# Optimization experiments

Measured on AMD Instinct MI355X. Metric: run time of the kernel, lower is better.

## Reference

```python
import jax, jax.numpy as jnp
import numpy as np


def setup_inputs() -> dict:
    key = jax.random.key(0)
    ks = jax.random.split(key, 9)
    B, C, O, T, H, W = 2, 256, 256, 16, 64, 64
    fea_th = jax.random.normal(ks[0], (B, C, T, H), dtype=jnp.float32)
    fea_tw = jax.random.normal(ks[1], (B, C, T, W), dtype=jnp.float32)
    fea_obj = jax.random.normal(ks[2], (B, C, T), dtype=jnp.float32)
    heatmap = jax.random.uniform(ks[3], (B, 1, T, H, W), dtype=jnp.float32)
    mask = jax.random.uniform(ks[4], (B, 1, T, H, W), dtype=jnp.float32)
    s = 1.0 / np.sqrt(C)
    W3d = jax.random.uniform(ks[5], (O, C), dtype=jnp.float32, minval=-s, maxval=s)
    b3d = jax.random.uniform(ks[6], (O,), dtype=jnp.float32, minval=-s, maxval=s)
    W1d = jax.random.uniform(ks[7], (O, C), dtype=jnp.float32, minval=-s, maxval=s)
    b1d = jax.random.uniform(ks[8], (O,), dtype=jnp.float32, minval=-s, maxval=s)
    return {"fea_th": fea_th, "fea_tw": fea_tw, "fea_obj": fea_obj,
            "heatmap": heatmap, "mask": mask,
            "W3d": W3d, "b3d": b3d, "W1d": W1d, "b1d": b1d}


def reference(fea_th, fea_tw, fea_obj, heatmap, mask, W3d, b3d, W1d, b1d):
    # Outer product over spatial dims: [B,C,T,H,1] * [B,C,T,1,W] -> [B,C,T,H,W]
    out_fea = fea_th[..., None] * fea_tw[..., None, :]
    # 1x1x1 Conv3d == channel mixing: bcthw,oc -> bothw (+ bias)
    out_fea = jnp.einsum('bcthw,oc->bothw', out_fea, W3d) + b3d[None, :, None, None, None]
    # 1x1 Conv1d on fea_obj: bct,oc -> bot (+ bias), then broadcast over H,W
    fea_obj_ = (jnp.einsum('bct,oc->bot', fea_obj, W1d) + b1d[None, :, None])[..., None, None]
    # Heatmap blend and mask
    out_fea = out_fea * (1.0 - heatmap) + fea_obj_ * heatmap
    out_fea = out_fea * mask
    return out_fea
```

## Files before the change

### kernel.cpp

```cpp
#include <hip/hip_runtime.h>
#include <hip/hip_bf16.h>

#define B_ 2
#define C_ 256
#define O_ 256
#define T_ 16
#define H_ 64
#define W_ 64

typedef __bf16 bf16x8 __attribute__((ext_vector_type(8)));
typedef float  f32x4  __attribute__((ext_vector_type(4)));

#define WS_OBJ_OFF 131072

__global__ __launch_bounds__(256) void prep_kernel(
    const float* __restrict__ fea_obj, const float* __restrict__ W3d,
    const float* __restrict__ W1d, const float* __restrict__ b1d,
    __bf16* __restrict__ wsW, float* __restrict__ wsObj) {
    const int bid = blockIdx.x;
    const int tid = threadIdx.x;
    if (bid < 32) {
        const int b = bid >> 4, t = bid & 15;
        __shared__ float fo[C_];
        fo[tid] = fea_obj[(b * C_ + tid) * T_ + t];
        __syncthreads();
        const int o = tid;
        const float4* wrow = (const float4*)(W1d + o * C_);
        float s = 0.f;
#pragma unroll 8
        for (int cq = 0; cq < C_ / 4; ++cq) {
            float4 wv = wrow[cq];
            s += wv.x * fo[cq * 4 + 0] + wv.y * fo[cq * 4 + 1] +
                 wv.z * fo[cq * 4 + 2] + wv.w * fo[cq * 4 + 3];
        }
        wsObj[(b * T_ + t) * O_ + o] = s + b1d[o];
    } else {
        const int g = (bid - 32) * 256 + tid;
        const int o = g >> 5;
        const int cg = g & 31;
        const float* sp = W3d + o * C_ + cg * 8;
        float4 a0 = *(const float4*)sp;
        float4 a1 = *(const float4*)(sp + 4);
        bf16x8 pk;
        pk[0] = (__bf16)a0.x; pk[1] = (__bf16)a0.y;
        pk[2] = (__bf16)a0.z; pk[3] = (__bf16)a0.w;
        pk[4] = (__bf16)a1.x; pk[5] = (__bf16)a1.y;
        pk[6] = (__bf16)a1.z; pk[7] = (__bf16)a1.w;
        *(bf16x8*)((char*)wsW + o * 512 + cg * 16) = pk;
    }
}

__global__ __attribute__((amdgpu_flat_work_group_size(512, 512)))
void main_kernel(
    const float* __restrict__ fea_th, const float* __restrict__ fea_tw,
    const float* __restrict__ heatmap, const float* __restrict__ mask,
    const float* __restrict__ b3d,
    const __bf16* __restrict__ wsW, const float* __restrict__ wsObj,
    float* __restrict__ out) {
    __shared__ __align__(16) char smem[43008];
    char*  sB0  = smem;
    char*  sB1  = smem + 16384;
    float* sTh  = (float*)(smem + 32768);
    float* sPb  = (float*)(smem + 40960);
    float* sObj = (float*)(smem + 41984);

    const int tid  = threadIdx.x;
    const int lane = tid & 63;
    const int wv   = tid >> 6;
    const int kgrp = lane >> 4;
    const int l15  = lane & 15;

    const int bid = blockIdx.x;
    const int wb = bid & 1, hg = (bid >> 1) & 7, bt = bid >> 4;
    const int b = bt >> 4, t = bt & 15;
    const int h0 = hg * 8, w0 = wb * 32;

    const float* objp = wsObj + (b * T_ + t) * O_;
    if (tid < 256) {
        const float* thp = fea_th + ((b * C_ + tid) * T_ + t) * H_ + h0;
        float4 v0 = *(const float4*)thp;
        float4 v1 = *(const float4*)(thp + 4);
        sTh[0 * 256 + tid] = v0.x;  sTh[1 * 256 + tid] = v0.y;
        sTh[2 * 256 + tid] = v0.z;  sTh[3 * 256 + tid] = v0.w;
        sTh[4 * 256 + tid] = v1.x;  sTh[5 * 256 + tid] = v1.y;
        sTh[6 * 256 + tid] = v1.z;  sTh[7 * 256 + tid] = v1.w;
        sPb[tid]  = b3d[tid];
        sObj[tid] = objp[tid];
    }

    const int wl = tid & 31;
    const int cs = (tid >> 5) * 16;
    bf16x8 twb0, twb1;
    {
        const float* twp = fea_tw + ((b * C_ + cs) * T_ + t) * W_ + w0 + wl;
#pragma unroll
        for (int j = 0; j < 8; ++j) twb0[j] = (__bf16)twp[j * (T_ * W_)];
#pragma unroll
        for (int j = 0; j < 8; ++j) twb1[j] = (__bf16)twp[(8 + j) * (T_ * W_)];
    }

    bf16x8 af[2][8];
#pragma unroll
    for (int mf = 0; mf < 2; ++mf)
#pragma unroll
        for (int ks = 0; ks < 8; ++ks)
            af[mf][ks] = *(const bf16x8*)(
                wsW + (wv * 32 + mf * 16 + l15) * 256 + ks * 32 + kgrp * 8);

    const int swzW = (wl & 7) << 4;
    const int c0g  = cs * 2;

    auto build = [&](int hl, char* dst) {
        const float* thp = sTh + hl * 256 + cs;
        const f32x4 t0 = *(const f32x4*)thp;
        const f32x4 t1 = *(const f32x4*)(thp + 4);
        const f32x4 t2 = *(const f32x4*)(thp + 8);
        const f32x4 t3 = *(const f32x4*)(thp + 12);
        bf16x8 z0, z1;
        z0[0] = (__bf16)((float)twb0[0] * t0[0]);
        z0[1] = (__bf16)((float)twb0[1] * t0[1]);
        z0[2] = (__bf16)((float)twb0[2] * t0[2]);
        z0[3] = (__bf16)((float)twb0[3] * t0[3]);
        z0[4] = (__bf16)((float)twb0[4] * t1[0]);
        z0[5] = (__bf16)((float)twb0[5] * t1[1]);
        z0[6] = (__bf16)((float)twb0[6] * t1[2]);
        z0[7] = (__bf16)((float)twb0[7] * t1[3]);
        z1[0] = (__bf16)((float)twb1[0] * t2[0]);
        z1[1] = (__bf16)((float)twb1[1] * t2[1]);
        z1[2] = (__bf16)((float)twb1[2] * t2[2]);
        z1[3] = (__bf16)((float)twb1[3] * t2[3]);
        z1[4] = (__bf16)((float)twb1[4] * t3[0]);
        z1[5] = (__bf16)((float)twb1[5] * t3[1]);
        z1[6] = (__bf16)((float)twb1[6] * t3[2]);
        z1[7] = (__bf16)((float)twb1[7] * t3[3]);
        *(bf16x8*)(dst + wl * 512 + (c0g ^ swzW))        = z0;
        *(bf16x8*)(dst + wl * 512 + ((c0g + 16) ^ swzW)) = z1;
    };

    __syncthreads();
    build(0, sB0);
    __syncthreads();

    const int hmb  = (b * T_ + t) * (H_ * W_);
    const int swzR = (l15 & 7) << 4;
    const int ob0  = wv * 32 + kgrp * 4;

    for (int hl = 0; hl < 8; ++hl) {
        char* cur = (hl & 1) ? sB1 : sB0;

        const int hglb = h0 + hl;
        const int hrow = hmb + hglb * W_ + w0 + l15;
        const float ht0 = heatmap[hrow],      mk0 = mask[hrow];
        const float ht1 = heatmap[hrow + 16], mk1 = mask[hrow + 16];

        f32x4 acc[2][2] = {};
#pragma unroll
        for (int ks = 0; ks < 8; ++ks) {
            const int kb = ks * 64 + kgrp * 16;
            const bf16x8 b0 = *(const bf16x8*)(cur + l15 * 512 + (kb ^ swzR));
            const bf16x8 b1 = *(const bf16x8*)(cur + (16 + l15) * 512 + (kb ^ swzR));
            acc[0][0] = __builtin_amdgcn_mfma_f32_16x16x32_bf16(af[0][ks], b0, acc[0][0], 0, 0, 0);
            acc[0][1] = __builtin_amdgcn_mfma_f32_16x16x32_bf16(af[0][ks], b1, acc[0][1], 0, 0, 0);
            acc[1][0] = __builtin_amdgcn_mfma_f32_16x16x32_bf16(af[1][ks], b0, acc[1][0], 0, 0, 0);
            acc[1][1] = __builtin_amdgcn_mfma_f32_16x16x32_bf16(af[1][ks], b1, acc[1][1], 0, 0, 0);
        }

        if (hl < 7) build(hl + 1, (hl & 1) ? sB0 : sB1);

        if (hl < 7) __syncthreads();

#pragma unroll
        for (int mf = 0; mf < 2; ++mf) {
            const f32x4 pb4 = *(const f32x4*)(sPb + ob0 + mf * 16);
            const f32x4 po4 = *(const f32x4*)(sObj + ob0 + mf * 16);
#pragma unroll
            for (int r = 0; r < 4; ++r) {
                const int o = ob0 + mf * 16 + r;
                float* orow = out + (((size_t)(b * O_ + o) * T_ + t) * H_ + hglb) * W_ + w0;
                float v0 = acc[mf][0][r] + pb4[r];
                v0 = v0 * (1.f - ht0) + po4[r] * ht0;
                orow[l15] = v0 * mk0;
                float v1 = acc[mf][1][r] + pb4[r];
                v1 = v1 * (1.f - ht1) + po4[r] * ht1;
                orow[16 + l15] = v1 * mk1;
            }
        }
    }
}

extern "C" void kernel_launch(void* const* d_in, const int* in_sizes, int n_in,
                              void* d_out, int out_size, void* d_ws, size_t ws_size,
                              hipStream_t stream) {
    const float* fea_th  = (const float*)d_in[0];
    const float* fea_tw  = (const float*)d_in[1];
    const float* fea_obj = (const float*)d_in[2];
    const float* heatmap = (const float*)d_in[3];
    const float* mask    = (const float*)d_in[4];
    const float* W3d     = (const float*)d_in[5];
    const float* b3d     = (const float*)d_in[6];
    const float* W1d     = (const float*)d_in[7];
    const float* b1d     = (const float*)d_in[8];
    float* out = (float*)d_out;

    __bf16* wsW  = (__bf16*)d_ws;
    float* wsObj = (float*)((char*)d_ws + WS_OBJ_OFF);

    hipLaunchKernelGGL(prep_kernel, dim3(64), dim3(256), 0, stream,
                       fea_obj, W3d, W1d, b1d, wsW, wsObj);
    hipLaunchKernelGGL(main_kernel, dim3(512), dim3(512), 0, stream,
                       fea_th, fea_tw, heatmap, mask, b3d, wsW, wsObj, out);
}
```

Before: 47.94 us.

## Process two H rows per barrier with k-major LDS layout for B tiles

```diff
diff --git a/kernel.cpp b/kernel.cpp
--- a/kernel.cpp
+++ b/kernel.cpp
@@ -57,12 +57,10 @@
     const float* __restrict__ b3d,
     const __bf16* __restrict__ wsW, const float* __restrict__ wsObj,
     float* __restrict__ out) {
-    __shared__ __align__(16) char smem[43008];
-    char*  sB0  = smem;
-    char*  sB1  = smem + 16384;
-    float* sTh  = (float*)(smem + 32768);
-    float* sPb  = (float*)(smem + 40960);
-    float* sObj = (float*)(smem + 41984);
+    __shared__ __align__(16) char smem[75776];
+    float* sTh  = (float*)(smem + 65536);
+    float* sPb  = (float*)(smem + 73728);
+    float* sObj = (float*)(smem + 74752);
 
     const int tid  = threadIdx.x;
     const int lane = tid & 63;
@@ -107,8 +105,8 @@
             af[mf][ks] = *(const bf16x8*)(
                 wsW + (wv * 32 + mf * 16 + l15) * 256 + ks * 32 + kgrp * 8);
 
-    const int swzW = (wl & 7) << 4;
-    const int c0g  = cs * 2;
+    const int wbyte = wl * 16;
+    const int cg0   = (tid >> 5) * 2;
 
     auto build = [&](int hl, char* dst) {
         const float* thp = sTh + hl * 256 + cs;
@@ -133,42 +131,44 @@
         z1[5] = (__bf16)((float)twb1[5] * t3[1]);
         z1[6] = (__bf16)((float)twb1[6] * t3[2]);
         z1[7] = (__bf16)((float)twb1[7] * t3[3]);
-        *(bf16x8*)(dst + wl * 512 + (c0g ^ swzW))        = z0;
-        *(bf16x8*)(dst + wl * 512 + ((c0g + 16) ^ swzW)) = z1;
+        *(bf16x8*)(dst + cg0 * 512 + wbyte)       = z0;
+        *(bf16x8*)(dst + (cg0 + 1) * 512 + wbyte) = z1;
     };
 
     __syncthreads();
-    build(0, sB0);
+    build(0, smem);
+    build(1, smem + 16384);
     __syncthreads();
 
-    const int hmb  = (b * T_ + t) * (H_ * W_);
-    const int swzR = (l15 & 7) << 4;
-    const int ob0  = wv * 32 + kgrp * 4;
-
-    for (int hl = 0; hl < 8; ++hl) {
-        char* cur = (hl & 1) ? sB1 : sB0;
-
-        const int hglb = h0 + hl;
-        const int hrow = hmb + hglb * W_ + w0 + l15;
-        const float ht0 = heatmap[hrow],      mk0 = mask[hrow];
-        const float ht1 = heatmap[hrow + 16], mk1 = mask[hrow + 16];
+    const int hmb = (b * T_ + t) * (H_ * W_);
+    const int ob0 = wv * 32 + kgrp * 4;
+    const int rb  = kgrp * 512 + l15 * 16;
+
+    for (int p = 0; p < 4; ++p) {
+        char* curA = smem + ((p & 1) ? 32768 : 0);
+        char* curB = curA + 16384;
+        char* nxtA = smem + ((p & 1) ? 0 : 32768);
+        char* nxtB = nxtA + 16384;
+        const int hA = h0 + 2 * p, hB = hA + 1;
+
+        const int rowA = hmb + hA * W_ + w0 + l15;
+        const int rowB = hmb + hB * W_ + w0 + l15;
+        const float htA0 = heatmap[rowA],      mkA0 = mask[rowA];
+        const float htA1 = heatmap[rowA + 16], mkA1 = mask[rowA + 16];
+        const float htB0 = heatmap[rowB],      mkB0 = mask[rowB];
+        const float htB1 = heatmap[rowB + 16], mkB1 = mask[rowB + 16];
 
         f32x4 acc[2][2] = {};
 #pragma unroll
         for (int ks = 0; ks < 8; ++ks) {
-            const int kb = ks * 64 + kgrp * 16;
-            const bf16x8 b0 = *(const bf16x8*)(cur + l15 * 512 + (kb ^ swzR));
-            const bf16x8 b1 = *(const bf16x8*)(cur + (16 + l15) * 512 + (kb ^ swzR));
+            const bf16x8 b0 = *(const bf16x8*)(curA + rb + ks * 2048);
+            const bf16x8 b1 = *(const bf16x8*)(curA + rb + ks * 2048 + 256);
             acc[0][0] = __builtin_amdgcn_mfma_f32_16x16x32_bf16(af[0][ks], b0, acc[0][0], 0, 0, 0);
             acc[0][1] = __builtin_amdgcn_mfma_f32_16x16x32_bf16(af[0][ks], b1, acc[0][1], 0, 0, 0);
             acc[1][0] = __builtin_amdgcn_mfma_f32_16x16x32_bf16(af[1][ks], b0, acc[1][0], 0, 0, 0);
             acc[1][1] = __builtin_amdgcn_mfma_f32_16x16x32_bf16(af[1][ks], b1, acc[1][1], 0, 0, 0);
         }
-
-        if (hl < 7) build(hl + 1, (hl & 1) ? sB0 : sB1);
-
-        if (hl < 7) __syncthreads();
-
+        if (p < 3) build(2 * p + 2, nxtA);
 #pragma unroll
         for (int mf = 0; mf < 2; ++mf) {
             const f32x4 pb4 = *(const f32x4*)(sPb + ob0 + mf * 16);
@@ -176,15 +176,45 @@
 #pragma unroll
             for (int r = 0; r < 4; ++r) {
                 const int o = ob0 + mf * 16 + r;
-                float* orow = out + (((size_t)(b * O_ + o) * T_ + t) * H_ + hglb) * W_ + w0;
+                float* orow = out + (((size_t)(b * O_ + o) * T_ + t) * H_ + hA) * W_ + w0;
                 float v0 = acc[mf][0][r] + pb4[r];
-                v0 = v0 * (1.f - ht0) + po4[r] * ht0;
-                orow[l15] = v0 * mk0;
+                v0 = v0 * (1.f - htA0) + po4[r] * htA0;
+                orow[l15] = v0 * mkA0;
                 float v1 = acc[mf][1][r] + pb4[r];
-                v1 = v1 * (1.f - ht1) + po4[r] * ht1;
-                orow[16 + l15] = v1 * mk1;
+                v1 = v1 * (1.f - htA1) + po4[r] * htA1;
+                orow[16 + l15] = v1 * mkA1;
             }
         }
+
+        f32x4 acd[2][2] = {};
+#pragma unroll
+        for (int ks = 0; ks < 8; ++ks) {
+            const bf16x8 b0 = *(const bf16x8*)(curB + rb + ks * 2048);
+            const bf16x8 b1 = *(const bf16x8*)(curB + rb + ks * 2048 + 256);
+            acd[0][0] = __builtin_amdgcn_mfma_f32_16x16x32_bf16(af[0][ks], b0, acd[0][0], 0, 0, 0);
+            acd[0][1] = __builtin_amdgcn_mfma_f32_16x16x32_bf16(af[0][ks], b1, acd[0][1], 0, 0, 0);
+            acd[1][0] = __builtin_amdgcn_mfma_f32_16x16x32_bf16(af[1][ks], b0, acd[1][0], 0, 0, 0);
+            acd[1][1] = __builtin_amdgcn_mfma_f32_16x16x32_bf16(af[1][ks], b1, acd[1][1], 0, 0, 0);
+        }
+        if (p < 3) build(2 * p + 3, nxtB);
+#pragma unroll
+        for (int mf = 0; mf < 2; ++mf) {
+            const f32x4 pb4 = *(const f32x4*)(sPb + ob0 + mf * 16);
+            const f32x4 po4 = *(const f32x4*)(sObj + ob0 + mf * 16);
+#pragma unroll
+            for (int r = 0; r < 4; ++r) {
+                const int o = ob0 + mf * 16 + r;
+                float* orow = out + (((size_t)(b * O_ + o) * T_ + t) * H_ + hB) * W_ + w0;
+                float v0 = acd[mf][0][r] + pb4[r];
+                v0 = v0 * (1.f - htB0) + po4[r] * htB0;
+                orow[l15] = v0 * mkB0;
+                float v1 = acd[mf][1][r] + pb4[r];
+                v1 = v1 * (1.f - htB1) + po4[r] * htB1;
+                orow[16 + l15] = v1 * mkB1;
+            }
+        }
+
+        if (p < 3) __syncthreads();
     }
 }
 
```

Measured after the change: 47.22 us. Within noise of the previous version (-1.5%).

## Split output channels across two blocks, K-major LDS layout, LDS-only barrier

Applied to the files above, without the earlier changes.

```diff
diff --git a/kernel.cpp b/kernel.cpp
--- a/kernel.cpp
+++ b/kernel.cpp
@@ -12,6 +12,12 @@
 typedef float  f32x4  __attribute__((ext_vector_type(4)));
 
 #define WS_OBJ_OFF 131072
+
+__device__ __forceinline__ void barrier_lds_only() {
+    asm volatile("s_waitcnt lgkmcnt(0)" ::: "memory");
+    __builtin_amdgcn_s_barrier();
+    asm volatile("" ::: "memory");
+}
 
 __global__ __launch_bounds__(256) void prep_kernel(
     const float* __restrict__ fea_obj, const float* __restrict__ W3d,
@@ -50,19 +56,18 @@
     }
 }
 
-__global__ __attribute__((amdgpu_flat_work_group_size(512, 512)))
+__global__ __attribute__((amdgpu_flat_work_group_size(512, 512),
+                          amdgpu_waves_per_eu(6)))
 void main_kernel(
     const float* __restrict__ fea_th, const float* __restrict__ fea_tw,
     const float* __restrict__ heatmap, const float* __restrict__ mask,
     const float* __restrict__ b3d,
     const __bf16* __restrict__ wsW, const float* __restrict__ wsObj,
     float* __restrict__ out) {
-    __shared__ __align__(16) char smem[43008];
-    char*  sB0  = smem;
-    char*  sB1  = smem + 16384;
+    __shared__ __align__(16) char smem[41984];
     float* sTh  = (float*)(smem + 32768);
     float* sPb  = (float*)(smem + 40960);
-    float* sObj = (float*)(smem + 41984);
+    float* sObj = (float*)(smem + 41472);
 
     const int tid  = threadIdx.x;
     const int lane = tid & 63;
@@ -71,9 +76,10 @@
     const int l15  = lane & 15;
 
     const int bid = blockIdx.x;
-    const int wb = bid & 1, hg = (bid >> 1) & 7, bt = bid >> 4;
+    const int mt = bid & 1, wb = (bid >> 1) & 1;
+    const int hg = (bid >> 2) & 7, bt = bid >> 5;
     const int b = bt >> 4, t = bt & 15;
-    const int h0 = hg * 8, w0 = wb * 32;
+    const int o0 = mt * 128, w0 = wb * 32, h0 = hg * 8;
 
     const float* objp = wsObj + (b * T_ + t) * O_;
     if (tid < 256) {
@@ -84,12 +90,15 @@
         sTh[2 * 256 + tid] = v0.z;  sTh[3 * 256 + tid] = v0.w;
         sTh[4 * 256 + tid] = v1.x;  sTh[5 * 256 + tid] = v1.y;
         sTh[6 * 256 + tid] = v1.z;  sTh[7 * 256 + tid] = v1.w;
-        sPb[tid]  = b3d[tid];
-        sObj[tid] = objp[tid];
+    } else if (tid < 384) {
+        const int i = tid - 256;
+        sPb[i]  = b3d[o0 + i];
+        sObj[i] = objp[o0 + i];
     }
 
     const int wl = tid & 31;
-    const int cs = (tid >> 5) * 16;
+    const int cr = tid >> 5;
+    const int cs = cr * 16;
     bf16x8 twb0, twb1;
     {
         const float* twp = fea_tw + ((b * C_ + cs) * T_ + t) * W_ + w0 + wl;
@@ -99,16 +108,13 @@
         for (int j = 0; j < 8; ++j) twb1[j] = (__bf16)twp[(8 + j) * (T_ * W_)];
     }
 
-    bf16x8 af[2][8];
-#pragma unroll
-    for (int mf = 0; mf < 2; ++mf)
-#pragma unroll
-        for (int ks = 0; ks < 8; ++ks)
-            af[mf][ks] = *(const bf16x8*)(
-                wsW + (wv * 32 + mf * 16 + l15) * 256 + ks * 32 + kgrp * 8);
-
-    const int swzW = (wl & 7) << 4;
-    const int c0g  = cs * 2;
+    bf16x8 af[8];
+#pragma unroll
+    for (int ks = 0; ks < 8; ++ks)
+        af[ks] = *(const bf16x8*)(
+            wsW + (o0 + wv * 16 + l15) * 256 + ks * 32 + kgrp * 8);
+
+    const int wbyte = wl * 16;
 
     auto build = [&](int hl, char* dst) {
         const float* thp = sTh + hl * 256 + cs;
@@ -133,57 +139,51 @@
         z1[5] = (__bf16)((float)twb1[5] * t3[1]);
         z1[6] = (__bf16)((float)twb1[6] * t3[2]);
         z1[7] = (__bf16)((float)twb1[7] * t3[3]);
-        *(bf16x8*)(dst + wl * 512 + (c0g ^ swzW))        = z0;
-        *(bf16x8*)(dst + wl * 512 + ((c0g + 16) ^ swzW)) = z1;
+        *(bf16x8*)(dst + (2 * cr) * 512 + wbyte)     = z0;
+        *(bf16x8*)(dst + (2 * cr + 1) * 512 + wbyte) = z1;
     };
 
     __syncthreads();
-    build(0, sB0);
+    build(0, smem);
     __syncthreads();
 
-    const int hmb  = (b * T_ + t) * (H_ * W_);
-    const int swzR = (l15 & 7) << 4;
-    const int ob0  = wv * 32 + kgrp * 4;
+    const int hmb = (b * T_ + t) * (H_ * W_);
+    const int ob  = wv * 16 + kgrp * 4;
+    const int rb  = kgrp * 512 + l15 * 16;
 
     for (int hl = 0; hl < 8; ++hl) {
-        char* cur = (hl & 1) ? sB1 : sB0;
+        char* cur = smem + ((hl & 1) ? 16384 : 0);
+        char* nxt = smem + ((hl & 1) ? 0 : 16384);
 
         const int hglb = h0 + hl;
         const int hrow = hmb + hglb * W_ + w0 + l15;
         const float ht0 = heatmap[hrow],      mk0 = mask[hrow];
         const float ht1 = heatmap[hrow + 16], mk1 = mask[hrow + 16];
 
-        f32x4 acc[2][2] = {};
+        f32x4 acc[2] = {};
 #pragma unroll
         for (int ks = 0; ks < 8; ++ks) {
-            const int kb = ks * 64 + kgrp * 16;
-            const bf16x8 b0 = *(const bf16x8*)(cur + l15 * 512 + (kb ^ swzR));
-            const bf16x8 b1 = *(const bf16x8*)(cur + (16 + l15) * 512 + (kb ^ swzR));
-            acc[0][0] = __builtin_amdgcn_mfma_f32_16x16x32_bf16(af[0][ks], b0, acc[0][0], 0, 0, 0);
-            acc[0][1] = __builtin_amdgcn_mfma_f32_16x16x32_bf16(af[0][ks], b1, acc[0][1], 0, 0, 0);
-            acc[1][0] = __builtin_amdgcn_mfma_f32_16x16x32_bf16(af[1][ks], b0, acc[1][0], 0, 0, 0);
-            acc[1][1] = __builtin_amdgcn_mfma_f32_16x16x32_bf16(af[1][ks], b1, acc[1][1], 0, 0, 0);
+            const bf16x8 b0 = *(const bf16x8*)(cur + rb + ks * 2048);
+            const bf16x8 b1 = *(const bf16x8*)(cur + rb + ks * 2048 + 256);
+            acc[0] = __builtin_amdgcn_mfma_f32_16x16x32_bf16(af[ks], b0, acc[0], 0, 0, 0);
+            acc[1] = __builtin_amdgcn_mfma_f32_16x16x32_bf16(af[ks], b1, acc[1], 0, 0, 0);
         }
 
-        if (hl < 7) build(hl + 1, (hl & 1) ? sB0 : sB1);
-
-        if (hl < 7) __syncthreads();
-
-#pragma unroll
-        for (int mf = 0; mf < 2; ++mf) {
-            const f32x4 pb4 = *(const f32x4*)(sPb + ob0 + mf * 16);
-            const f32x4 po4 = *(const f32x4*)(sObj + ob0 + mf * 16);
-#pragma unroll
-            for (int r = 0; r < 4; ++r) {
-                const int o = ob0 + mf * 16 + r;
-                float* orow = out + (((size_t)(b * O_ + o) * T_ + t) * H_ + hglb) * W_ + w0;
-                float v0 = acc[mf][0][r] + pb4[r];
-                v0 = v0 * (1.f - ht0) + po4[r] * ht0;
-                orow[l15] = v0 * mk0;
-                float v1 = acc[mf][1][r] + pb4[r];
-                v1 = v1 * (1.f - ht1) + po4[r] * ht1;
-                orow[16 + l15] = v1 * mk1;
-            }
+        if (hl < 7) build(hl + 1, nxt);
+        if (hl < 7) barrier_lds_only();
+
+        const f32x4 pb4 = *(const f32x4*)(sPb + ob);
+        const f32x4 po4 = *(const f32x4*)(sObj + ob);
+#pragma unroll
+        for (int r = 0; r < 4; ++r) {
+            const int o = o0 + ob + r;
+            float* orow = out + (((size_t)(b * O_ + o) * T_ + t) * H_ + hglb) * W_ + w0;
+            float v0 = acc[0][r] + pb4[r];
+            v0 = v0 * (1.f - ht0) + po4[r] * ht0;
+            orow[l15] = v0 * mk0;
+            float v1 = acc[1][r] + pb4[r];
+            v1 = v1 * (1.f - ht1) + po4[r] * ht1;
+            orow[16 + l15] = v1 * mk1;
         }
     }
 }
@@ -207,6 +207,6 @@
 
     hipLaunchKernelGGL(prep_kernel, dim3(64), dim3(256), 0, stream,
                        fea_obj, W3d, W1d, b1d, wsW, wsObj);
-    hipLaunchKernelGGL(main_kernel, dim3(512), dim3(512), 0, stream,
+    hipLaunchKernelGGL(main_kernel, dim3(1024), dim3(512), 0, stream,
                        fea_th, fea_tw, heatmap, mask, b3d, wsW, wsObj, out);
 }
```

Result: slower. 54.44 us (+13.6%).
